# Kernel tuning notes

Measured on AMD Instinct MI355X. Metric: run time of the kernel, lower is better.

The kernel has to match this reference:

```python
import jax, jax.numpy as jnp
import numpy as np

B, D, P, OUT = 16384, 1024, 1024, 25


def setup_inputs() -> dict:
    key = jax.random.key(0)
    ks = jax.random.split(key, 8)
    return {
        "patient_embed": jax.random.normal(ks[0], (B, D), jnp.float32),
        "prototype_embed": jax.random.normal(ks[1], (P, D), jnp.float32),
        "index": jax.random.permutation(ks[2], B),
        "bilinear_w": jax.random.normal(ks[3], (1, D, D), jnp.float32) * 0.02,
        "bilinear_b": jnp.zeros((1,), jnp.float32),
        "lin_w": jax.random.normal(ks[4], (1, 2 * D), jnp.float32) * 0.02,
        "proto_fc_w": jax.random.normal(ks[5], (P, D), jnp.float32) * 0.02,
        "proto_fc_b": jnp.zeros((P,), jnp.float32),
        "class_fc_w": jax.random.normal(ks[6], (OUT, P), jnp.float32) * 0.02,
        "class_fc_b": jnp.zeros((OUT,), jnp.float32),
    }


def reference(patient_embed, prototype_embed, index, bilinear_w, bilinear_b,
              lin_w, proto_fc_w, proto_fc_b, class_fc_w, class_fc_b):
    # prototype codebook is detached in the original (clone().detach())
    protos = jax.lax.stop_gradient(prototype_embed)  # [P, D]

    # cdist + argmin: nearest prototype per patient (VQ-style codebook lookup)
    e_sq = jnp.sum(patient_embed * patient_embed, axis=-1, keepdims=True)  # [B,1]
    p_sq = jnp.sum(protos * protos, axis=-1)[None, :]                      # [1,P]
    d2 = e_sq + p_sq - 2.0 * (patient_embed @ protos.T)                    # [B,P]
    dist = jnp.sqrt(jnp.maximum(d2, 0.0))
    labels_a = jnp.argmin(dist, axis=1)                                    # [B]

    # mixup partner via permutation; its nearest prototype is a gather of labels_a
    embed_b = patient_embed[index]
    labels_b = labels_a[index]

    pa = protos[labels_a]  # [B, D] prototype gather
    pb = protos[labels_b]

    # BiaffineAttention: bilinear(pa, pb) + lin(cat(pa, pb))
    bil = jnp.einsum('bi,oij,bj->bo', pa, bilinear_w, pb) + bilinear_b     # [B,1]
    lin = jnp.concatenate([pa, pb], axis=1) @ lin_w.T                      # [B,1]
    lam = jax.nn.sigmoid(bil + lin)                                        # [B,1]

    # adaptive mixup blend
    mixed_embed = lam * patient_embed + (1.0 - lam) * embed_b              # [B,D]

    # class_linear(mixed_embed) = class_fc(leaky_relu(proto_fc(mixed_embed)))
    proto_logits = mixed_embed @ proto_fc_w.T + proto_fc_b                 # [B,P]
    cls_logits = jax.nn.leaky_relu(proto_logits, 0.01) @ class_fc_w.T + class_fc_b  # [B,OUT]
    return cls_logits
```

## Files before the change

kernel.cpp:

```cpp
#include <hip/hip_runtime.h>
#include <math.h>

#define B_   16384
#define D_   1024
#define P_   1024
#define KS_  2048
#define OUT_ 25
#define NT_  48

typedef unsigned short u16;
typedef unsigned int   u32;
typedef unsigned long long u64;
typedef __attribute__((ext_vector_type(8))) short short8;
typedef __attribute__((ext_vector_type(4))) float f32x4;
typedef _Float16 half_t;
typedef __attribute__((ext_vector_type(2))) _Float16 h2;

struct alignas(8) U16x4 { u16 x, y, z, w; };
struct alignas(8) H4 { half_t x, y, z, w; };
struct alignas(16) H8 { h2 a, b, c, d; };

#if defined(__has_builtin)
#if __has_builtin(__builtin_amdgcn_fdot2)
#define HAS_FDOT2 1
#endif
#endif

#define SBAR()   __builtin_amdgcn_s_barrier()
#define WAITV0() asm volatile("s_waitcnt vmcnt(0)" ::: "memory")
#define PRIO1()  __builtin_amdgcn_s_setprio(1)
#define PRIO0()  __builtin_amdgcn_s_setprio(0)

__device__ __forceinline__ u16 f2bf(float f) {
  u32 u = __float_as_uint(f);
  u32 r = (u + 0x7FFFu + ((u >> 16) & 1u)) >> 16;
  return (u16)r;
}
__device__ __forceinline__ float bf2f(u16 h) {
  return __uint_as_float(((u32)h) << 16);
}
__device__ __forceinline__ u32 ordkey(float f) {
  u32 u = __float_as_uint(f);
  return (u & 0x80000000u) ? ~u : (u | 0x80000000u);
}
__device__ __forceinline__ void gload_lds16(const u16* g, u16* l) {
  __builtin_amdgcn_global_load_lds(
      (const __attribute__((address_space(1))) u32*)g,
      (__attribute__((address_space(3))) u32*)l, 16, 0, 0);
}
__device__ __forceinline__ float dot8(const H8& a, const H8& b, float c) {
#ifdef HAS_FDOT2
  c = __builtin_amdgcn_fdot2(a.a, b.a, c, false);
  c = __builtin_amdgcn_fdot2(a.b, b.b, c, false);
  c = __builtin_amdgcn_fdot2(a.c, b.c, c, false);
  c = __builtin_amdgcn_fdot2(a.d, b.d, c, false);
#else
  c += (float)a.a.x * (float)b.a.x + (float)a.a.y * (float)b.a.y;
  c += (float)a.b.x * (float)b.b.x + (float)a.b.y * (float)b.b.y;
  c += (float)a.c.x * (float)b.c.x + (float)a.c.y * (float)b.c.y;
  c += (float)a.d.x * (float)b.d.x + (float)a.d.y * (float)b.d.y;
#endif
  return c;
}
__device__ __forceinline__ int wrapNT(int t) { return t >= NT_ ? t - NT_ : t; }
__device__ __forceinline__ int acolf(int t) { t = wrapNT(t); return ((t >> 4) == 1 ? 1024 : 0) + (t & 15) * 64; }
__device__ __forceinline__ int bcolf(int t) { t = wrapNT(t); return ((t >> 4) == 2 ? 1024 : 0) + (t & 15) * 64; }


__global__ void conv_split(const float* __restrict__ in, u16* __restrict__ out) {
  int r = blockIdx.x, t = threadIdx.x;
  float4 x = ((const float4*)(in + (size_t)r * D_))[t];
  U16x4 h, l;
  h.x = f2bf(x.x); l.x = f2bf(x.x - bf2f(h.x));
  h.y = f2bf(x.y); l.y = f2bf(x.y - bf2f(h.y));
  h.z = f2bf(x.z); l.z = f2bf(x.z - bf2f(h.z));
  h.w = f2bf(x.w); l.w = f2bf(x.w - bf2f(h.w));
  u16* o = out + (size_t)r * KS_ + t * 4;
  *(U16x4*)(o)      = h;
  *(U16x4*)(o + D_) = l;
}

__global__ void convProtos(const float* __restrict__ protos, const float* __restrict__ lin_w,
                           u16* __restrict__ p2,
                           float* __restrict__ psq, float* __restrict__ uu, float* __restrict__ vv) {
  int r = blockIdx.x, t = threadIdx.x;
  float4 x  = ((const float4*)(protos + (size_t)r * D_))[t];
  float4 w1 = ((const float4*)(lin_w))[t];
  float4 w2 = ((const float4*)(lin_w + D_))[t];
  U16x4 h, l;
  h.x = f2bf(x.x); l.x = f2bf(x.x - bf2f(h.x));
  h.y = f2bf(x.y); l.y = f2bf(x.y - bf2f(h.y));
  h.z = f2bf(x.z); l.z = f2bf(x.z - bf2f(h.z));
  h.w = f2bf(x.w); l.w = f2bf(x.w - bf2f(h.w));
  u16* o = p2 + (size_t)r * KS_ + t * 4;
  *(U16x4*)(o) = h; *(U16x4*)(o + D_) = l;

  float s1 = x.x*x.x + x.y*x.y + x.z*x.z + x.w*x.w;
  float s2 = x.x*w1.x + x.y*w1.y + x.z*w1.z + x.w*w1.w;
  float s3 = x.x*w2.x + x.y*w2.y + x.z*w2.z + x.w*w2.w;
  #pragma unroll
  for (int mk = 1; mk < 64; mk <<= 1) {
    s1 += __shfl_xor(s1, mk);
    s2 += __shfl_xor(s2, mk);
    s3 += __shfl_xor(s3, mk);
  }
  __shared__ float r1[4], r2[4], r3[4];
  if ((t & 63) == 0) { int w = t >> 6; r1[w] = s1; r2[w] = s2; r3[w] = s3; }
  __syncthreads();
  if (t == 0) {
    psq[r] = r1[0] + r1[1] + r1[2] + r1[3];
    uu[r]  = r2[0] + r2[1] + r2[2] + r2[3];
    vv[r]  = r3[0] + r3[1] + r3[2] + r3[3];
  }
}

__global__ void convWt(const float* __restrict__ W, u16* __restrict__ wt2) {
  __shared__ float tile[64][65];
  int bx = blockIdx.x, by = blockIdx.y;
  int t = threadIdx.x;
  int c4 = (t & 15) * 4, r0 = t >> 4;
  #pragma unroll
  for (int rr = 0; rr < 64; rr += 16) {
    int r = rr + r0;
    float4 x = *(const float4*)(W + (size_t)(bx * 64 + r) * D_ + by * 64 + c4);
    tile[r][c4 + 0] = x.x; tile[r][c4 + 1] = x.y; tile[r][c4 + 2] = x.z; tile[r][c4 + 3] = x.w;
  }
  __syncthreads();
  #pragma unroll
  for (int rr = 0; rr < 64; rr += 16) {
    int r = rr + r0;
    U16x4 h, l;
    float v0 = tile[c4 + 0][r], v1 = tile[c4 + 1][r], v2 = tile[c4 + 2][r], v3 = tile[c4 + 3][r];
    h.x = f2bf(v0); l.x = f2bf(v0 - bf2f(h.x));
    h.y = f2bf(v1); l.y = f2bf(v1 - bf2f(h.y));
    h.z = f2bf(v2); l.z = f2bf(v2 - bf2f(h.z));
    h.w = f2bf(v3); l.w = f2bf(v3 - bf2f(h.w));
    u16* o = wt2 + (size_t)(by * 64 + r) * KS_ + bx * 64 + c4;
    *(U16x4*)(o) = h; *(U16x4*)(o + D_) = l;
  }
}

#define MFMAQ(MH, AF, BQ, O)                                                     \
  {                                                                              \
    _Pragma("unroll")                                                            \
    for (int mi = 0; mi < 4; ++mi) {                                             \
      _Pragma("unroll")                                                          \
      for (int nj = 0; nj < 4; ++nj)                                             \
        acc[(MH) * 4 + mi][nj] = __builtin_amdgcn_mfma_f32_16x16x32_bf16(        \
            (AF)[mi], (BQ)[(O) + nj], acc[(MH) * 4 + mi][nj], 0, 0, 0);          \
    }                                                                            \
  }

template<int MODE>
__global__ __launch_bounds__(512, 2) void gemm256(
    const u16* __restrict__ A, const u16* __restrict__ Bm,
    u16* __restrict__ Ch,
    const float* __restrict__ psq, u64* __restrict__ packed,
    const float* __restrict__ bias)
{
  extern __shared__ u16 lds[];
  int bid = blockIdx.x;
  int wg = ((bid & 7) << 5) + (bid >> 3);
  int tm = wg >> 2, tn = wg & 3;
  int m0 = tm << 8, n0 = tn << 8;

  int tid = threadIdx.x;
  int w = tid >> 6, lane = tid & 63;
  int wm = w >> 2, wn = w & 3;
  int lr = lane & 15, lg = lane >> 4;

  #define AOFF(kkh, buf) (((kkh) * 2 + (buf)) * 8192)

  auto stage = [&](int row0, int colbase, int dstoff) {
    #pragma unroll
    for (int q = 0; q < 2; ++q) {
      int r = q * 128 + w * 16 + (lane >> 2);
      int c = ((lane & 3) * 8) ^ (((r >> 3) & 1) << 4);
      gload_lds16(A + (size_t)(row0 + r) * KS_ + colbase + c,
                  &lds[dstoff + q * 4096 + w * 512]);
    }
  };
  auto lda = [&](int kkh, int buf, int mh, short8* dst) {
    const u16* Asl = &lds[AOFF(kkh, buf)];
    #pragma unroll
    for (int mi = 0; mi < 4; ++mi) {
      int r = wm * 128 + mh * 64 + mi * 16 + lr;
      dst[mi] = *(const short8*)&Asl[r * 32 + ((lg * 8) ^ (((r >> 3) & 1) << 4))];
    }
  };
  const u16* browbase = Bm + (size_t)(n0 + wn * 64 + lr) * KS_ + lg * 8;
  auto loadB = [&](int t, short8* dst) {
    int cb = bcolf(t);
    #pragma unroll
    for (int kkh = 0; kkh < 2; ++kkh)
      #pragma unroll
      for (int nj = 0; nj < 4; ++nj)
        dst[kkh * 4 + nj] =
            *(const short8*)(browbase + (size_t)(nj * 16) * KS_ + cb + kkh * 32);
  };

  f32x4 acc[8][4];
  #pragma unroll
  for (int i = 0; i < 8; ++i)
    #pragma unroll
    for (int j = 0; j < 4; ++j)
      acc[i][j] = (f32x4){0.f, 0.f, 0.f, 0.f};

  short8 af[4], bqA[8], bqB[8];

  stage(m0, acolf(0) +  0, AOFF(0, 0));
  stage(m0, acolf(0) + 32, AOFF(1, 0));
  loadB(0, bqA);
  WAITV0();

  #define TILEBODY(T, BUF, NBUF, BQC, BQN)                                      \
  {                                                                             \
    SBAR();                                                                     \
    stage(m0, acolf((T) + 1) +  0, AOFF(0, NBUF));                              \
    stage(m0, acolf((T) + 1) + 32, AOFF(1, NBUF));                              \
    loadB((T) + 1, BQN);                                                        \
    lda(0, BUF, 0, af);                                                         \
    PRIO1(); MFMAQ(0, af, BQC, 0); PRIO0();                                     \
    lda(0, BUF, 1, af);                                                         \
    PRIO1(); MFMAQ(1, af, BQC, 0); PRIO0();                                     \
    lda(1, BUF, 0, af);                                                         \
    PRIO1(); MFMAQ(0, af, BQC, 4); PRIO0();                                     \
    lda(1, BUF, 1, af);                                                         \
    PRIO1(); MFMAQ(1, af, BQC, 4); PRIO0();                                     \
    WAITV0();                                                                   \
  }

  for (int t = 0; t < NT_; t += 2) {
    TILEBODY(t,     0, 1, bqA, bqB);
    TILEBODY(t + 1, 1, 0, bqB, bqA);
  }
  #undef TILEBODY

  if (MODE == 1) {
    float pq[4];
    #pragma unroll
    for (int nj = 0; nj < 4; ++nj) pq[nj] = psq[n0 + wn * 64 + nj * 16 + lr];
    #pragma unroll
    for (int mi = 0; mi < 8; ++mi) {
      #pragma unroll
      for (int r = 0; r < 4; ++r) {
        float best = 1e30f; int bestn = 0x7fffffff;
        #pragma unroll
        for (int nj = 0; nj < 4; ++nj) {
          int n = n0 + wn * 64 + nj * 16 + lr;
          float d = pq[nj] - 2.0f * acc[mi][nj][r];
          if (d < best || (d == best && n < bestn)) { best = d; bestn = n; }
        }
        #pragma unroll
        for (int mk = 1; mk < 16; mk <<= 1) {
          float od = __shfl_xor(best, mk);
          int   on = __shfl_xor(bestn, mk);
          if (od < best || (od == best && on < bestn)) { best = od; bestn = on; }
        }
        if (lr == 0) {
          int m = m0 + wm * 128 + mi * 16 + lg * 4 + r;
          u64 key = ((u64)ordkey(best) << 32) | (u32)bestn;
          atomicMin(&packed[m], key);
        }
      }
    }
  } else {
    float bc[4];
    #pragma unroll
    for (int nj = 0; nj < 4; ++nj) bc[nj] = bias[n0 + wn * 64 + nj * 16 + lr];
    #pragma unroll
    for (int mi = 0; mi < 8; ++mi)
      #pragma unroll
      for (int nj = 0; nj < 4; ++nj)
        #pragma unroll
        for (int r = 0; r < 4; ++r) {
          int m = m0 + wm * 128 + mi * 16 + lg * 4 + r;
          int n = n0 + wn * 64 + nj * 16 + lr;
          float val = acc[mi][nj][r] + bc[nj];
          val = val >= 0.f ? val : 0.01f * val;
          half_t hv = (half_t)val;
          Ch[(size_t)m * P_ + n] = __builtin_bit_cast(u16, hv);
        }
  }
  #undef AOFF
}

__global__ __launch_bounds__(256) void gemm_T_splitk(
    const u16* __restrict__ A, const u16* __restrict__ Bm, float* __restrict__ Cp)
{
  __shared__ u16 As[128 * 32];
  __shared__ u16 Bs[128 * 32];

  int bid = blockIdx.x;
  int swz = (bid & 7) * 24 + (bid >> 3);
  int kp = swz >> 6;
  int wg = swz & 63;
  int tm = wg >> 3, tn = wg & 7;
  int m0 = tm * 128, n0 = tn * 128;
  int abase = (kp == 1) ? 1024 : 0;
  int bbase = (kp == 2) ? 1024 : 0;

  int t = threadIdx.x;
  int w = t >> 6, lane = t & 63;
  int wr = w >> 1, wc = w & 1;
  int lr = lane & 15, lg = lane >> 4;

  const u16* src = (w < 2) ? A : Bm;
  int base_row = (w < 2) ? m0 : n0;
  int kbase = (w < 2) ? abase : bbase;
  int half = w & 1;
  int srow = base_row + half * 64 + (lane >> 2);
  int scol = (lane & 3) * 8;
  const u16* gsrc = src + (size_t)srow * KS_ + kbase + scol;
  u16* lbase = ((w < 2) ? As : Bs) + half * 2048;

  f32x4 acc[4][4];
  #pragma unroll
  for (int i = 0; i < 4; ++i)
    #pragma unroll
    for (int j = 0; j < 4; ++j)
      acc[i][j] = (f32x4){0.f, 0.f, 0.f, 0.f};

  for (int kt = 0; kt < 32; ++kt) {
    #pragma unroll
    for (int p = 0; p < 4; ++p)
      gload_lds16(gsrc + kt * 32 + (size_t)p * 16 * KS_, lbase + p * 512);
    __syncthreads();
    short8 af[4], bfr[4];
    #pragma unroll
    for (int i = 0; i < 4; ++i)
      af[i] = *(const short8*)&As[(wr * 64 + i * 16 + lr) * 32 + lg * 8];
    #pragma unroll
    for (int j = 0; j < 4; ++j)
      bfr[j] = *(const short8*)&Bs[(wc * 64 + j * 16 + lr) * 32 + lg * 8];
    #pragma unroll
    for (int i = 0; i < 4; ++i)
      #pragma unroll
      for (int j = 0; j < 4; ++j)
        acc[i][j] = __builtin_amdgcn_mfma_f32_16x16x32_bf16(af[i], bfr[j], acc[i][j], 0, 0, 0);
    __syncthreads();
  }

  float* Co = Cp + (size_t)kp * (P_ * D_);
  #pragma unroll
  for (int i = 0; i < 4; ++i)
    #pragma unroll
    for (int j = 0; j < 4; ++j)
      #pragma unroll
      for (int r = 0; r < 4; ++r) {
        int m = m0 + wr * 64 + i * 16 + lg * 4 + r;
        int n = n0 + wc * 64 + j * 16 + lr;
        Co[(size_t)m * D_ + n] = acc[i][j][r];
      }
}

__global__ void mix_kernel(const u64* __restrict__ packed, const int* __restrict__ index,
                           const float* __restrict__ Tp, const float* __restrict__ protos,
                           const float* __restrict__ patient,
                           const float* __restrict__ uu, const float* __restrict__ vv,
                           const float* __restrict__ bilb, u16* __restrict__ mixed2)
{
  int b = blockIdx.x, t = threadIdx.x;
  int la = (int)(packed[b] & 0xffffffffULL);
  int ib = index[b];
  int lb = (int)(packed[ib] & 0xffffffffULL);

  float4 t0 = ((const float4*)(Tp + (size_t)la * D_))[t];
  float4 t1 = ((const float4*)(Tp + (size_t)(P_ * D_) + (size_t)la * D_))[t];
  float4 t2 = ((const float4*)(Tp + (size_t)(2 * P_ * D_) + (size_t)la * D_))[t];
  float4 pb = ((const float4*)(protos + (size_t)lb * D_))[t];
  float tax = t0.x + t1.x + t2.x, tay = t0.y + t1.y + t2.y;
  float taz = t0.z + t1.z + t2.z, taw = t0.w + t1.w + t2.w;
  float part = tax*pb.x + tay*pb.y + taz*pb.z + taw*pb.w;
  #pragma unroll
  for (int mk = 1; mk < 64; mk <<= 1) part += __shfl_xor(part, mk);
  __shared__ float ws4[4];
  __shared__ float lamsh;
  if ((t & 63) == 0) ws4[t >> 6] = part;
  __syncthreads();
  if (t == 0) {
    float dot = ws4[0] + ws4[1] + ws4[2] + ws4[3];
    float z = dot + bilb[0] + uu[la] + vv[lb];
    lamsh = 1.0f / (1.0f + expf(-z));
  }
  __syncthreads();
  float lam = lamsh, oml = 1.0f - lam;

  float4 xa = ((const float4*)(patient + (size_t)b  * D_))[t];
  float4 xb = ((const float4*)(patient + (size_t)ib * D_))[t];
  float m0v = lam * xa.x + oml * xb.x;
  float m1v = lam * xa.y + oml * xb.y;
  float m2v = lam * xa.z + oml * xb.z;
  float m3v = lam * xa.w + oml * xb.w;
  U16x4 h, l;
  h.x = f2bf(m0v); l.x = f2bf(m0v - bf2f(h.x));
  h.y = f2bf(m1v); l.y = f2bf(m1v - bf2f(h.y));
  h.z = f2bf(m2v); l.z = f2bf(m2v - bf2f(h.z));
  h.w = f2bf(m3v); l.w = f2bf(m3v - bf2f(h.w));
  u16* o = mixed2 + (size_t)b * KS_ + t * 4;
  *(U16x4*)(o) = h; *(U16x4*)(o + D_) = l;
}

__global__ __launch_bounds__(256) void cls_kernel(const u16* __restrict__ pl,
                                                  const float* __restrict__ w,
                                                  const float* __restrict__ bias,
                                                  float* __restrict__ out)
{
  __shared__ half_t wl[25 * 1032];
  int t = threadIdx.x;
  for (int i = t; i < 25 * 256; i += 256) {
    float4 v = ((const float4*)w)[i];
    int o = i >> 8;
    int col = (i & 255) * 4;
    H4 hh; hh.x = (half_t)v.x; hh.y = (half_t)v.y; hh.z = (half_t)v.z; hh.w = (half_t)v.w;
    *(H4*)&wl[o * 1032 + col] = hh;
  }
  __syncthreads();

  int row = blockIdx.x * 64 + (t >> 2);
  int osub = t & 3;
  const H8* prow = (const H8*)(pl + (size_t)row * P_);
  float acc[7] = {0.f, 0.f, 0.f, 0.f, 0.f, 0.f, 0.f};

  for (int kk = 0; kk < 128; ++kk) {
    H8 a = prow[kk];
    #pragma unroll
    for (int j = 0; j < 7; ++j) {
      int o = 4 * j + osub;
      if (o < 25) {
        H8 wv = *(const H8*)&wl[o * 1032 + kk * 8];
        acc[j] = dot8(a, wv, acc[j]);
      }
    }
  }
  #pragma unroll
  for (int j = 0; j < 7; ++j) {
    int o = 4 * j + osub;
    if (o < 25) out[(size_t)row * OUT_ + o] = acc[j] + bias[o];
  }
}

extern "C" void kernel_launch(void* const* d_in, const int* in_sizes, int n_in,
                              void* d_out, int out_size, void* d_ws, size_t ws_size,
                              hipStream_t stream)
{
  const float* patient = (const float*)d_in[0];
  const float* protos  = (const float*)d_in[1];
  const int*   index   = (const int*)d_in[2];
  const float* W       = (const float*)d_in[3];
  const float* bilb    = (const float*)d_in[4];
  const float* lin_w   = (const float*)d_in[5];
  const float* pfc_w   = (const float*)d_in[6];
  const float* pfc_b   = (const float*)d_in[7];
  const float* cls_w   = (const float*)d_in[8];
  const float* cls_b   = (const float*)d_in[9];
  float* out = (float*)d_out;

  char* ws = (char*)d_ws;
  size_t off = 0;
  auto carve = [&](size_t bytes) -> char* {
    char* p = ws + off; off += (bytes + 255) & ~(size_t)255; return p;
  };
  u16* buf2   = (u16*)carve((size_t)B_ * KS_ * 2);
  u16* plh    = (u16*)carve((size_t)B_ * P_ * 2);
  u16* p2     = (u16*)carve((size_t)P_ * KS_ * 2);
  u16* pfc2   = (u16*)carve((size_t)P_ * KS_ * 2);
  u16* wt2    = (u16*)carve((size_t)D_ * KS_ * 2);
  float* Tp   = (float*)carve((size_t)3 * P_ * D_ * 4);
  u64* packed = (u64*)carve((size_t)B_ * 8);
  float* psq  = (float*)carve(P_ * 4);
  float* uu   = (float*)carve(P_ * 4);
  float* vv   = (float*)carve(P_ * 4);

  hipMemsetAsync(packed, 0xFF, (size_t)B_ * 8, stream);

  convProtos<<<P_, 256, 0, stream>>>(protos, lin_w, p2, psq, uu, vv);
  convWt<<<dim3(16, 16), 256, 0, stream>>>(W, wt2);
  conv_split<<<P_, 256, 0, stream>>>(pfc_w, pfc2);
  conv_split<<<B_, 256, 0, stream>>>(patient, buf2);

  gemm_T_splitk<<<192, 256, 0, stream>>>(p2, wt2, Tp);
  gemm256<1><<<256, 512, 65536, stream>>>(buf2, p2, nullptr, psq, packed, nullptr);
  mix_kernel<<<B_, 256, 0, stream>>>(packed, index, Tp, protos, patient, uu, vv, bilb, buf2);
  gemm256<2><<<256, 512, 65536, stream>>>(buf2, pfc2, plh, nullptr, nullptr, pfc_b);
  cls_kernel<<<256, 256, 0, stream>>>(plh, cls_w, cls_b, out);
}
```

Baseline: 534.8 us.

## Restructure GEMM main loop with single B buffer and partial vmcnt waits

Replaces the double-buffered B register fragments with one buffer that is reloaded at the end of each tile, after the MFMAs. A-fragment LDS reads are split into two alternating register sets so the next LDS read can overlap the current MFMAs. The full vmcnt(0) wait becomes a partial vmcnt(12) wait before a barrier, so only the A staging for the current buffer has to land. This frees VGPRs and may loosen the sync, but it adds a second barrier per tile and leaves the B global loads with little work to hide behind before the next tile needs them.

```diff
diff --git a/kernel.cpp b/kernel.cpp
--- a/kernel.cpp
+++ b/kernel.cpp
@@ -26,10 +26,11 @@
 #endif
 #endif
 
-#define SBAR()   __builtin_amdgcn_s_barrier()
-#define WAITV0() asm volatile("s_waitcnt vmcnt(0)" ::: "memory")
-#define PRIO1()  __builtin_amdgcn_s_setprio(1)
-#define PRIO0()  __builtin_amdgcn_s_setprio(0)
+#define SBAR()    __builtin_amdgcn_s_barrier()
+#define WAITV12() asm volatile("s_waitcnt vmcnt(12)" ::: "memory")
+#define WAITV0()  asm volatile("s_waitcnt vmcnt(0)" ::: "memory")
+#define PRIO1()   __builtin_amdgcn_s_setprio(1)
+#define PRIO0()   __builtin_amdgcn_s_setprio(0)
 
 __device__ __forceinline__ u16 f2bf(float f) {
   u32 u = __float_as_uint(f);
@@ -140,14 +141,14 @@
   }
 }
 
-#define MFMAQ(MH, AF, BQ, O)                                                     \
+#define MFMAQ(MH, AF, O)                                                         \
   {                                                                              \
     _Pragma("unroll")                                                            \
     for (int mi = 0; mi < 4; ++mi) {                                             \
       _Pragma("unroll")                                                          \
       for (int nj = 0; nj < 4; ++nj)                                             \
         acc[(MH) * 4 + mi][nj] = __builtin_amdgcn_mfma_f32_16x16x32_bf16(        \
-            (AF)[mi], (BQ)[(O) + nj], acc[(MH) * 4 + mi][nj], 0, 0, 0);          \
+            (AF)[mi], bq[(O) + nj], acc[(MH) * 4 + mi][nj], 0, 0, 0);            \
     }                                                                            \
   }
 
@@ -189,13 +190,14 @@
     }
   };
   const u16* browbase = Bm + (size_t)(n0 + wn * 64 + lr) * KS_ + lg * 8;
-  auto loadB = [&](int t, short8* dst) {
+  short8 bq[8];
+  auto loadB = [&](int t) {
     int cb = bcolf(t);
     #pragma unroll
     for (int kkh = 0; kkh < 2; ++kkh)
       #pragma unroll
       for (int nj = 0; nj < 4; ++nj)
-        dst[kkh * 4 + nj] =
+        bq[kkh * 4 + nj] =
             *(const short8*)(browbase + (size_t)(nj * 16) * KS_ + cb + kkh * 32);
   };
 
@@ -206,35 +208,38 @@
     for (int j = 0; j < 4; ++j)
       acc[i][j] = (f32x4){0.f, 0.f, 0.f, 0.f};
 
-  short8 af[4], bqA[8], bqB[8];
+  short8 afA[4], afB[4];
 
   stage(m0, acolf(0) +  0, AOFF(0, 0));
   stage(m0, acolf(0) + 32, AOFF(1, 0));
-  loadB(0, bqA);
+  loadB(0);
   WAITV0();
-
-  #define TILEBODY(T, BUF, NBUF, BQC, BQN)                                      \
+  SBAR();
+
+  #define TILEBODY(T, BUF, NBUF)                                                \
   {                                                                             \
-    SBAR();                                                                     \
     stage(m0, acolf((T) + 1) +  0, AOFF(0, NBUF));                              \
     stage(m0, acolf((T) + 1) + 32, AOFF(1, NBUF));                              \
-    loadB((T) + 1, BQN);                                                        \
-    lda(0, BUF, 0, af);                                                         \
-    PRIO1(); MFMAQ(0, af, BQC, 0); PRIO0();                                     \
-    lda(0, BUF, 1, af);                                                         \
-    PRIO1(); MFMAQ(1, af, BQC, 0); PRIO0();                                     \
-    lda(1, BUF, 0, af);                                                         \
-    PRIO1(); MFMAQ(0, af, BQC, 4); PRIO0();                                     \
-    lda(1, BUF, 1, af);                                                         \
-    PRIO1(); MFMAQ(1, af, BQC, 4); PRIO0();                                     \
-    WAITV0();                                                                   \
+    WAITV12();                                                                  \
+    SBAR();                                                                     \
+    lda(0, BUF, 0, afA);                                                        \
+    lda(0, BUF, 1, afB);                                                        \
+    PRIO1(); MFMAQ(0, afA, 0); PRIO0();                                         \
+    lda(1, BUF, 0, afA);                                                        \
+    PRIO1(); MFMAQ(1, afB, 0); PRIO0();                                         \
+    lda(1, BUF, 1, afB);                                                        \
+    PRIO1(); MFMAQ(0, afA, 4); PRIO0();                                         \
+    PRIO1(); MFMAQ(1, afB, 4); PRIO0();                                         \
+    loadB((T) + 1);                                                             \
+    SBAR();                                                                     \
   }
 
   for (int t = 0; t < NT_; t += 2) {
-    TILEBODY(t,     0, 1, bqA, bqB);
-    TILEBODY(t + 1, 1, 0, bqB, bqA);
+    TILEBODY(t,     0, 1);
+    TILEBODY(t + 1, 1, 0);
   }
   #undef TILEBODY
+  WAITV0();
 
   if (MODE == 1) {
     float pq[4];
```

Result: no change. 532.7 us (-0.4%).
